# Kernel tuning notes

Hardware: AMD Instinct MI355X
Metric: run time of the kernel (lower is better)

Reference implementation:

```python
import jax, jax.numpy as jnp
import numpy as np


def _graph_conv(x, W, b, src, dst, norm_src, norm_dst, n_nodes):
    # DGL GraphConv, norm='both': out = D_in^{-1/2} * A * D_out^{-1/2} * x * W + b
    h = x * norm_src[:, None]                      # [N, d] scale by src out-degree norm
    m = h[src]                                     # [E, d] gather (irregular access)
    agg = jax.ops.segment_sum(m, dst, num_segments=n_nodes)  # [N, d] scatter-add
    agg = agg * norm_dst[:, None]
    return agg @ W + b


def setup_inputs() -> dict:
    key = jax.random.key(0)
    ks = jax.random.split(key, 6)
    N, E, IN, HID = 50000, 800000, 64, 128
    in_feat = jax.random.normal(ks[0], (N, IN), dtype=jnp.float32)
    W1 = jax.random.normal(ks[1], (IN, HID), dtype=jnp.float32) * (1.0 / np.sqrt(IN))
    b1 = jnp.zeros((HID,), dtype=jnp.float32)
    W2 = jax.random.normal(ks[2], (HID, IN), dtype=jnp.float32) * (1.0 / np.sqrt(HID))
    b2 = jnp.zeros((IN,), dtype=jnp.float32)
    src = jax.random.randint(ks[3], (E,), 0, N, dtype=jnp.int32)
    dst = jax.random.randint(ks[4], (E,), 0, N, dtype=jnp.int32)
    return {"in_feat": in_feat, "W1": W1, "b1": b1, "W2": W2, "b2": b2,
            "src": src, "dst": dst, "n_nodes": N}


def reference(in_feat, W1, b1, W2, b2, src, dst, n_nodes):
    ones = jnp.ones(src.shape, dtype=in_feat.dtype)
    deg_out = jax.ops.segment_sum(ones, src, num_segments=n_nodes)
    deg_in = jax.ops.segment_sum(ones, dst, num_segments=n_nodes)
    # DGL clamps degrees to min 1 (allow_zero_in_degree=True just skips the check)
    norm_src = jnp.clip(deg_out, 1.0, None) ** -0.5
    norm_dst = jnp.clip(deg_in, 1.0, None) ** -0.5
    h = _graph_conv(in_feat, W1, b1, src, dst, norm_src, norm_dst, n_nodes)
    h = jax.nn.relu(h)
    h = _graph_conv(h, W2, b2, src, dst, norm_src, norm_dst, n_nodes)
    return h
```

## Files before the change

### kernel.cpp

```cpp
#include <hip/hip_runtime.h>

#define IN_F 64
#define HID_F 128
#define CAP 64
#define CHUNK 4096
#define CAPB 4096
#define MAXB 512

typedef unsigned short u16;
typedef unsigned int u32;
typedef _Float16 f16;
typedef __attribute__((ext_vector_type(4))) _Float16 f16x4;
typedef __attribute__((ext_vector_type(8))) _Float16 f16x8;
typedef __attribute__((ext_vector_type(4))) float f32x4;

__global__ __launch_bounds__(256)
void partition_kernel(const int* __restrict__ src, const int* __restrict__ dst,
                      int* __restrict__ gcurD, int* __restrict__ gcurS,
                      u32* __restrict__ bufD, u16* __restrict__ bufS,
                      const float* __restrict__ W1, const float* __restrict__ W2,
                      f16* __restrict__ W1t, f16* __restrict__ W2t,
                      int E, int NBUCK) {
    if (blockIdx.x == gridDim.x - 1) {
        for (int t = threadIdx.x; t < 2 * IN_F * HID_F; t += 256) {
            if (t < IN_F * HID_F) {
                int n = t / IN_F, k = t % IN_F;
                W1t[t] = (f16)W1[k * HID_F + n];
            } else {
                int i = t - IN_F * HID_F;
                int n = i / HID_F, k = i % HID_F;
                W2t[i] = (f16)W2[k * IN_F + n];
            }
        }
        return;
    }
    __shared__ int histD[MAXB], histS[MAXB], baseD[MAXB], baseS[MAXB];
    const int t  = threadIdx.x;
    const int e0 = blockIdx.x * CHUNK;
    const int n  = min(CHUNK, E - e0);

    int ed[16], es[16];

    for (int b = t; b < NBUCK; b += 256) { histD[b] = 0; histS[b] = 0; }
    __syncthreads();
#pragma unroll
    for (int j = 0; j < 16; ++j) {
        int i = t + j * 256;
        if (i < n) {
            ed[j] = dst[e0 + i];
            es[j] = src[e0 + i];
            atomicAdd(&histD[ed[j] >> 7], 1);
            atomicAdd(&histS[es[j] >> 7], 1);
        }
    }
    __syncthreads();
    for (int b = t; b < NBUCK; b += 256) {
        baseD[b] = atomicAdd(&gcurD[b], histD[b]);
        baseS[b] = atomicAdd(&gcurS[b], histS[b]);
        histD[b] = 0;
        histS[b] = 0;
    }
    __syncthreads();
#pragma unroll
    for (int j = 0; j < 16; ++j) {
        int i = t + j * 256;
        if (i < n) {
            int d  = ed[j];
            int s  = es[j];
            int bD = d >> 7, bS = s >> 7;
            int p  = baseD[bD] + atomicAdd(&histD[bD], 1);
            if (p < CAPB) bufD[(size_t)bD * CAPB + p] = (u32)d | ((u32)s << 16);
            int p2 = baseS[bS] + atomicAdd(&histS[bS], 1);
            if (p2 < CAPB) bufS[(size_t)bS * CAPB + p2] = (u16)s;
        }
    }
}

__global__ __launch_bounds__(256)
void bucket_pass2_kernel(const u32* __restrict__ bufD, const int* __restrict__ gcurD,
                         const u16* __restrict__ bufS, const int* __restrict__ gcurS,
                         u16* __restrict__ slots, int* __restrict__ deg_in,
                         float* __restrict__ norm_dst, float* __restrict__ norm_src,
                         const float* __restrict__ x, f16x4* __restrict__ scaled_x,
                         int N, int NBUCK) {
    __shared__ int lcur[128];
    const int t = threadIdx.x;
    if (t < 128) lcur[t] = 0;
    __syncthreads();
    if (blockIdx.x < NBUCK) {
        const int b = blockIdx.x;
        const int cnt = min(gcurD[b], CAPB);
        const u32* p = bufD + (size_t)b * CAPB;
        for (int i = t; i < cnt; i += 256) {
            u32 v = p[i];
            int d = (int)(v & 0xFFFFu);
            int s = (int)(v >> 16);
            int pos = atomicAdd(&lcur[d & 127], 1);
            if (pos < CAP) slots[(size_t)d * CAP + pos] = (u16)s;
        }
        __syncthreads();
        int node = b * 128 + t;
        if (t < 128 && node < N) {
            deg_in[node]   = lcur[t];
            norm_dst[node] = rsqrtf((float)max(lcur[t], 1));
        }
    } else {
        const int b = blockIdx.x - NBUCK;
        const int cnt = min(gcurS[b], CAPB);
        const u16* p = bufS + (size_t)b * CAPB;
        for (int i = t; i < cnt; i += 256)
            atomicAdd(&lcur[p[i] & 127], 1);
        __syncthreads();
        int node0 = b * 128;
        if (t < 128 && node0 + t < N)
            norm_src[node0 + t] = rsqrtf((float)max(lcur[t], 1));
        for (int i = t; i < 128 * 16; i += 256) {
            int r = i >> 4, c = i & 15;
            int node = node0 + r;
            if (node < N) {
                float ns = rsqrtf((float)max(lcur[r], 1));
                float4 v = ((const float4*)x)[(size_t)node * 16 + c];
                f16x4 h;
                h.x = (f16)(v.x * ns); h.y = (f16)(v.y * ns);
                h.z = (f16)(v.z * ns); h.w = (f16)(v.w * ns);
                scaled_x[(size_t)node * 16 + c] = h;
            }
        }
    }
}

__global__ __launch_bounds__(256)
void gather_gemm_kernel(const f16x8* __restrict__ xs, const u16* __restrict__ slots,
                        const int* __restrict__ deg_in,
                        const f16* __restrict__ W1t, const float* __restrict__ b1,
                        const float* __restrict__ nd, const float* __restrict__ ns,
                        const f16* __restrict__ W2t, f16* __restrict__ g2, int N) {
    constexpr int LDX = IN_F + 8;
    constexpr int LDH = HID_F + 8;
    __shared__ __align__(16) f16 sx[32 * LDX];
    __shared__ __align__(16) f16 h[2][16 * LDH];

    const int t   = threadIdx.x;
    const int row = t >> 3;
    const int c   = t & 7;
    const int r0  = blockIdx.x * 32;
    const int node = r0 + row;

    float acc[8];
#pragma unroll
    for (int k = 0; k < 8; ++k) acc[k] = 0.f;
    if (node < N) {
        int deg = min(deg_in[node], CAP);
        const u16* srow = slots + (size_t)node * CAP;
        int i = 0;
        for (; i + 8 <= deg; i += 8) {
            int s[8];
#pragma unroll
            for (int j = 0; j < 8; ++j) s[j] = (int)srow[i + j];
            f16x8 v[8];
#pragma unroll
            for (int j = 0; j < 8; ++j) v[j] = xs[(size_t)s[j] * 8 + c];
#pragma unroll
            for (int j = 0; j < 8; ++j)
#pragma unroll
                for (int k = 0; k < 8; ++k) acc[k] += (float)v[j][k];
        }
        for (; i < deg; ++i) {
            f16x8 v = xs[(size_t)srow[i] * 8 + c];
#pragma unroll
            for (int k = 0; k < 8; ++k) acc[k] += (float)v[k];
        }
    }
    {
        f16x8 hv;
#pragma unroll
        for (int k = 0; k < 8; ++k) hv[k] = (f16)acc[k];
        *(f16x8*)&sx[row * LDX + c * 8] = hv;
    }
    __syncthreads();

    const int wave = t >> 6;
    const int lane = t & 63;
    const int nl   = lane & 15;
    const int quad = lane >> 4;

#pragma unroll
    for (int rt = 0; rt < 2; ++rt) {
        f16x8 a1[2];
#pragma unroll
        for (int kf = 0; kf < 2; ++kf)
            a1[kf] = *(const f16x8*)(sx + (rt * 16 + nl) * LDX + kf * 32 + quad * 8);

        float rs1[4];
#pragma unroll
        for (int reg = 0; reg < 4; ++reg)
            rs1[reg] = nd[min(r0 + rt * 16 + quad * 4 + reg, N - 1)];

        f16* hb = h[rt];
#pragma unroll
        for (int cti = 0; cti < 2; ++cti) {
            const int ct = wave * 2 + cti;
            f32x4 acc1 = (f32x4){0.f, 0.f, 0.f, 0.f};
#pragma unroll
            for (int kf = 0; kf < 2; ++kf) {
                f16x8 b = *(const f16x8*)(W1t + (ct * 16 + nl) * IN_F + kf * 32 + quad * 8);
                acc1 = __builtin_amdgcn_mfma_f32_16x16x32_f16(a1[kf], b, acc1, 0, 0, 0);
            }
            float bb = b1[ct * 16 + nl];
#pragma unroll
            for (int reg = 0; reg < 4; ++reg) {
                float v = fmaxf(acc1[reg] * rs1[reg] + bb, 0.f);
                hb[(quad * 4 + reg) * LDH + ct * 16 + nl] = (f16)v;
            }
        }
    }
    __syncthreads();

#pragma unroll
    for (int rt = 0; rt < 2; ++rt) {
        f32x4 acc2 = (f32x4){0.f, 0.f, 0.f, 0.f};
#pragma unroll
        for (int kf = 0; kf < 4; ++kf) {
            f16x8 a2 = *(const f16x8*)(h[rt] + nl * LDH + kf * 32 + quad * 8);
            f16x8 b  = *(const f16x8*)(W2t + (wave * 16 + nl) * HID_F + kf * 32 + quad * 8);
            acc2 = __builtin_amdgcn_mfma_f32_16x16x32_f16(a2, b, acc2, 0, 0, 0);
        }

        float rs2[4];
#pragma unroll
        for (int reg = 0; reg < 4; ++reg)
            rs2[reg] = ns[min(r0 + rt * 16 + quad * 4 + reg, N - 1)];
#pragma unroll
        for (int reg = 0; reg < 4; ++reg) {
            int r = r0 + rt * 16 + quad * 4 + reg;
            if (r < N)
                g2[(size_t)r * IN_F + wave * 16 + nl] = (f16)(acc2[reg] * rs2[reg]);
        }
    }
}

__global__ __launch_bounds__(256)
void gather_out_kernel(const f16x8* __restrict__ xs, const u16* __restrict__ slots,
                       const int* __restrict__ deg_in, const float* __restrict__ sd,
                       const float* __restrict__ bias,
                       float4* __restrict__ out, int N) {
    int tg = blockIdx.x * blockDim.x + threadIdx.x;
    int node = tg >> 3;
    int c = tg & 7;
    if (node >= N) return;
    int deg = min(deg_in[node], CAP);
    const u16* srow = slots + (size_t)node * CAP;
    float acc[8];
#pragma unroll
    for (int k = 0; k < 8; ++k) acc[k] = 0.f;

    int i = 0;
    for (; i + 8 <= deg; i += 8) {
        int s[8];
#pragma unroll
        for (int j = 0; j < 8; ++j) s[j] = (int)srow[i + j];
        f16x8 v[8];
#pragma unroll
        for (int j = 0; j < 8; ++j) v[j] = xs[(size_t)s[j] * 8 + c];
#pragma unroll
        for (int j = 0; j < 8; ++j)
#pragma unroll
            for (int k = 0; k < 8; ++k) acc[k] += (float)v[j][k];
    }
    for (; i < deg; ++i) {
        f16x8 v = xs[(size_t)srow[i] * 8 + c];
#pragma unroll
        for (int k = 0; k < 8; ++k) acc[k] += (float)v[k];
    }
    float d = sd[node];
    float4 b0 = ((const float4*)bias)[c * 2];
    float4 b1v = ((const float4*)bias)[c * 2 + 1];
    float4 o0, o1;
    o0.x = acc[0] * d + b0.x;  o0.y = acc[1] * d + b0.y;
    o0.z = acc[2] * d + b0.z;  o0.w = acc[3] * d + b0.w;
    o1.x = acc[4] * d + b1v.x; o1.y = acc[5] * d + b1v.y;
    o1.z = acc[6] * d + b1v.z; o1.w = acc[7] * d + b1v.w;
    out[(size_t)node * 16 + c * 2]     = o0;
    out[(size_t)node * 16 + c * 2 + 1] = o1;
}

extern "C" void kernel_launch(void* const* d_in, const int* in_sizes, int n_in,
                              void* d_out, int out_size, void* d_ws, size_t ws_size,
                              hipStream_t stream) {
    const float* in_feat = (const float*)d_in[0];
    const float* W1      = (const float*)d_in[1];
    const float* b1      = (const float*)d_in[2];
    const float* W2      = (const float*)d_in[3];
    const float* b2      = (const float*)d_in[4];
    const int*   src     = (const int*)d_in[5];
    const int*   dst     = (const int*)d_in[6];

    const int N = in_sizes[0] / IN_F;
    const int E = in_sizes[5];
    float* out = (float*)d_out;

    const int NBUCK = (N + 127) >> 7;

    int* deg_in  = (int*)d_ws;
    int* gcurD   = deg_in + N;
    int* gcurS   = gcurD + MAXB;
    u16* slots   = (u16*)(gcurS + MAXB);
    float* norm_src = (float*)(slots + (size_t)N * CAP);
    float* norm_dst = norm_src + N;
    f16* scaled_x = (f16*)(norm_dst + N);
    f16* g2       = scaled_x + (size_t)N * IN_F;
    f16* W1t      = g2 + (size_t)N * IN_F;
    f16* W2t      = W1t + IN_F * HID_F;
    u32* bufD     = (u32*)(W2t + IN_F * HID_F);
    u16* bufS     = (u16*)(bufD + (size_t)NBUCK * CAPB);

    hipMemsetAsync(gcurD, 0, sizeof(int) * 2 * MAXB, stream);
    partition_kernel<<<(E + CHUNK - 1) / CHUNK + 1, 256, 0, stream>>>(
        src, dst, gcurD, gcurS, bufD, bufS, W1, W2, W1t, W2t, E, NBUCK);

    bucket_pass2_kernel<<<2 * NBUCK, 256, 0, stream>>>(
        bufD, gcurD, bufS, gcurS, slots, deg_in, norm_dst, norm_src,
        in_feat, (f16x4*)scaled_x, N, NBUCK);

    gather_gemm_kernel<<<(N + 31) / 32, 256, 0, stream>>>(
        (const f16x8*)scaled_x, slots, deg_in, W1t, b1, norm_dst, norm_src,
        W2t, g2, N);

    gather_out_kernel<<<(N * 8 + 255) / 256, 256, 0, stream>>>(
        (const f16x8*)g2, slots, deg_in, norm_dst, b2, (float4*)out, N);
}
```

Before: 167.6 us.

## Replace two-pass bucket partition with direct global-atomic adjacency build

Replaces the bucketed partition and second pass (LDS histograms, staging buffers, bucket scatter) with a single kernel that does global atomicAdd on per-node degree counters and writes the source index straight into the per-destination slot list. A separate prep kernel then computes the norms, writes the scaled fp16 features and transposes the weights. This removes the staging buffers and one full pass over the edges, but adds many contended global atomics with random addresses. Slot order within each node becomes nondeterministic, so fp16 accumulation order varies from run to run.

New measurement: 219.0 us. 1.31x slower.

```diff
diff --git a/kernel.cpp b/kernel.cpp
--- a/kernel.cpp
+++ b/kernel.cpp
@@ -3,9 +3,6 @@
 #define IN_F 64
 #define HID_F 128
 #define CAP 64
-#define CHUNK 4096
-#define CAPB 4096
-#define MAXB 512
 
 typedef unsigned short u16;
 typedef unsigned int u32;
@@ -15,12 +12,39 @@
 typedef __attribute__((ext_vector_type(4))) float f32x4;
 
 __global__ __launch_bounds__(256)
-void partition_kernel(const int* __restrict__ src, const int* __restrict__ dst,
-                      int* __restrict__ gcurD, int* __restrict__ gcurS,
-                      u32* __restrict__ bufD, u16* __restrict__ bufS,
-                      const float* __restrict__ W1, const float* __restrict__ W2,
-                      f16* __restrict__ W1t, f16* __restrict__ W2t,
-                      int E, int NBUCK) {
+void build_kernel(const int* __restrict__ src, const int* __restrict__ dst,
+                  int* __restrict__ deg_in, int* __restrict__ deg_out,
+                  u16* __restrict__ slots, int E) {
+    const int q = blockIdx.x * 256 + threadIdx.x;
+    const int i0 = q * 4;
+    if (i0 + 3 < E) {
+        int4 d4 = ((const int4*)dst)[q];
+        int4 s4 = ((const int4*)src)[q];
+        int dd[4] = {d4.x, d4.y, d4.z, d4.w};
+        int ss[4] = {s4.x, s4.y, s4.z, s4.w};
+#pragma unroll
+        for (int j = 0; j < 4; ++j) {
+            int pos = atomicAdd(&deg_in[dd[j]], 1);
+            if (pos < CAP) slots[(size_t)dd[j] * CAP + pos] = (u16)ss[j];
+            atomicAdd(&deg_out[ss[j]], 1);
+        }
+    } else {
+        for (int i = i0; i < E; ++i) {
+            int d = dst[i], s = src[i];
+            int pos = atomicAdd(&deg_in[d], 1);
+            if (pos < CAP) slots[(size_t)d * CAP + pos] = (u16)s;
+            atomicAdd(&deg_out[s], 1);
+        }
+    }
+}
+
+__global__ __launch_bounds__(256)
+void prep_kernel(const float* __restrict__ x, const int* __restrict__ deg_in,
+                 const int* __restrict__ deg_out,
+                 float* __restrict__ norm_dst, float* __restrict__ norm_src,
+                 f16x8* __restrict__ scaled_x,
+                 const float* __restrict__ W1, const float* __restrict__ W2,
+                 f16* __restrict__ W1t, f16* __restrict__ W2t, int N) {
     if (blockIdx.x == gridDim.x - 1) {
         for (int t = threadIdx.x; t < 2 * IN_F * HID_F; t += 256) {
             if (t < IN_F * HID_F) {
@@ -34,99 +58,23 @@
         }
         return;
     }
-    __shared__ int histD[MAXB], histS[MAXB], baseD[MAXB], baseS[MAXB];
-    const int t  = threadIdx.x;
-    const int e0 = blockIdx.x * CHUNK;
-    const int n  = min(CHUNK, E - e0);
-
-    int ed[16], es[16];
-
-    for (int b = t; b < NBUCK; b += 256) { histD[b] = 0; histS[b] = 0; }
-    __syncthreads();
-#pragma unroll
-    for (int j = 0; j < 16; ++j) {
-        int i = t + j * 256;
-        if (i < n) {
-            ed[j] = dst[e0 + i];
-            es[j] = src[e0 + i];
-            atomicAdd(&histD[ed[j] >> 7], 1);
-            atomicAdd(&histS[es[j] >> 7], 1);
-        }
-    }
-    __syncthreads();
-    for (int b = t; b < NBUCK; b += 256) {
-        baseD[b] = atomicAdd(&gcurD[b], histD[b]);
-        baseS[b] = atomicAdd(&gcurS[b], histS[b]);
-        histD[b] = 0;
-        histS[b] = 0;
-    }
-    __syncthreads();
-#pragma unroll
-    for (int j = 0; j < 16; ++j) {
-        int i = t + j * 256;
-        if (i < n) {
-            int d  = ed[j];
-            int s  = es[j];
-            int bD = d >> 7, bS = s >> 7;
-            int p  = baseD[bD] + atomicAdd(&histD[bD], 1);
-            if (p < CAPB) bufD[(size_t)bD * CAPB + p] = (u32)d | ((u32)s << 16);
-            int p2 = baseS[bS] + atomicAdd(&histS[bS], 1);
-            if (p2 < CAPB) bufS[(size_t)bS * CAPB + p2] = (u16)s;
-        }
-    }
-}
-
-__global__ __launch_bounds__(256)
-void bucket_pass2_kernel(const u32* __restrict__ bufD, const int* __restrict__ gcurD,
-                         const u16* __restrict__ bufS, const int* __restrict__ gcurS,
-                         u16* __restrict__ slots, int* __restrict__ deg_in,
-                         float* __restrict__ norm_dst, float* __restrict__ norm_src,
-                         const float* __restrict__ x, f16x4* __restrict__ scaled_x,
-                         int N, int NBUCK) {
-    __shared__ int lcur[128];
-    const int t = threadIdx.x;
-    if (t < 128) lcur[t] = 0;
-    __syncthreads();
-    if (blockIdx.x < NBUCK) {
-        const int b = blockIdx.x;
-        const int cnt = min(gcurD[b], CAPB);
-        const u32* p = bufD + (size_t)b * CAPB;
-        for (int i = t; i < cnt; i += 256) {
-            u32 v = p[i];
-            int d = (int)(v & 0xFFFFu);
-            int s = (int)(v >> 16);
-            int pos = atomicAdd(&lcur[d & 127], 1);
-            if (pos < CAP) slots[(size_t)d * CAP + pos] = (u16)s;
-        }
-        __syncthreads();
-        int node = b * 128 + t;
-        if (t < 128 && node < N) {
-            deg_in[node]   = lcur[t];
-            norm_dst[node] = rsqrtf((float)max(lcur[t], 1));
-        }
-    } else {
-        const int b = blockIdx.x - NBUCK;
-        const int cnt = min(gcurS[b], CAPB);
-        const u16* p = bufS + (size_t)b * CAPB;
-        for (int i = t; i < cnt; i += 256)
-            atomicAdd(&lcur[p[i] & 127], 1);
-        __syncthreads();
-        int node0 = b * 128;
-        if (t < 128 && node0 + t < N)
-            norm_src[node0 + t] = rsqrtf((float)max(lcur[t], 1));
-        for (int i = t; i < 128 * 16; i += 256) {
-            int r = i >> 4, c = i & 15;
-            int node = node0 + r;
-            if (node < N) {
-                float ns = rsqrtf((float)max(lcur[r], 1));
-                float4 v = ((const float4*)x)[(size_t)node * 16 + c];
-                f16x4 h;
-                h.x = (f16)(v.x * ns); h.y = (f16)(v.y * ns);
-                h.z = (f16)(v.z * ns); h.w = (f16)(v.w * ns);
-                scaled_x[(size_t)node * 16 + c] = h;
-            }
-        }
-    }
+    const int t = blockIdx.x * 256 + threadIdx.x;
+    const int node = t >> 3;
+    const int c = t & 7;
+    if (node >= N) return;
+    float nsv = rsqrtf((float)max(deg_out[node], 1));
+    if (c == 0) {
+        norm_src[node] = nsv;
+        norm_dst[node] = rsqrtf((float)max(deg_in[node], 1));
+    }
+    float4 a = ((const float4*)x)[(size_t)node * 16 + c * 2];
+    float4 b = ((const float4*)x)[(size_t)node * 16 + c * 2 + 1];
+    f16x8 h;
+    h[0] = (f16)(a.x * nsv); h[1] = (f16)(a.y * nsv);
+    h[2] = (f16)(a.z * nsv); h[3] = (f16)(a.w * nsv);
+    h[4] = (f16)(b.x * nsv); h[5] = (f16)(b.y * nsv);
+    h[6] = (f16)(b.z * nsv); h[7] = (f16)(b.w * nsv);
+    scaled_x[(size_t)node * 8 + c] = h;
 }
 
 __global__ __launch_bounds__(256)
@@ -299,28 +247,23 @@
     const int E = in_sizes[5];
     float* out = (float*)d_out;
 
-    const int NBUCK = (N + 127) >> 7;
-
-    int* deg_in  = (int*)d_ws;
-    int* gcurD   = deg_in + N;
-    int* gcurS   = gcurD + MAXB;
-    u16* slots   = (u16*)(gcurS + MAXB);
+    int* deg_in   = (int*)d_ws;
+    int* deg_out  = deg_in + N;
+    u16* slots    = (u16*)(deg_out + N);
     float* norm_src = (float*)(slots + (size_t)N * CAP);
     float* norm_dst = norm_src + N;
     f16* scaled_x = (f16*)(norm_dst + N);
     f16* g2       = scaled_x + (size_t)N * IN_F;
     f16* W1t      = g2 + (size_t)N * IN_F;
     f16* W2t      = W1t + IN_F * HID_F;
-    u32* bufD     = (u32*)(W2t + IN_F * HID_F);
-    u16* bufS     = (u16*)(bufD + (size_t)NBUCK * CAPB);
-
-    hipMemsetAsync(gcurD, 0, sizeof(int) * 2 * MAXB, stream);
-    partition_kernel<<<(E + CHUNK - 1) / CHUNK + 1, 256, 0, stream>>>(
-        src, dst, gcurD, gcurS, bufD, bufS, W1, W2, W1t, W2t, E, NBUCK);
-
-    bucket_pass2_kernel<<<2 * NBUCK, 256, 0, stream>>>(
-        bufD, gcurD, bufS, gcurS, slots, deg_in, norm_dst, norm_src,
-        in_feat, (f16x4*)scaled_x, N, NBUCK);
+
+    hipMemsetAsync(deg_in, 0, sizeof(int) * 2 * N, stream);
+    build_kernel<<<(E / 4 + 255) / 256, 256, 0, stream>>>(
+        src, dst, deg_in, deg_out, slots, E);
+
+    prep_kernel<<<(N * 8 + 255) / 256 + 1, 256, 0, stream>>>(
+        in_feat, deg_in, deg_out, norm_dst, norm_src,
+        (f16x8*)scaled_x, W1, W2, W1t, W2t, N);
 
     gather_gemm_kernel<<<(N + 31) / 32, 256, 0, stream>>>(
         (const f16x8*)scaled_x, slots, deg_in, W1t, b1, norm_dst, norm_src,
```

## Split feature gathers into column halves to shrink random-access working set

Applied to the files above, without the earlier changes.

Stores scaled_x and g2 in a column-split layout of two 32-wide fp16 halves, each contiguous over nodes. Each gather now runs as two passes, one per half, so the randomly accessed table per pass is half the size and more likely to stay in cache. The first layer writes a float32 partial aggregate to a new workspace buffer between passes, and the second layer's output is produced by two kernel launches. Nontemporal loads and stores are used on streamed slots and outputs to keep them from evicting the gathered table, at the cost of reading the slot lists twice and paying extra launches and intermediate traffic.

New measurement: 192.7 us. 1.15x slower.

```diff
diff --git a/kernel.cpp b/kernel.cpp
--- a/kernel.cpp
+++ b/kernel.cpp
@@ -115,26 +115,61 @@
         if (t < 128 && node0 + t < N)
             norm_src[node0 + t] = rsqrtf((float)max(lcur[t], 1));
         for (int i = t; i < 128 * 16; i += 256) {
-            int r = i >> 4, c = i & 15;
+            int r = i >> 4, cc = i & 15;
             int node = node0 + r;
             if (node < N) {
                 float ns = rsqrtf((float)max(lcur[r], 1));
-                float4 v = ((const float4*)x)[(size_t)node * 16 + c];
+                float4 v = ((const float4*)x)[(size_t)node * 16 + cc];
                 f16x4 h;
                 h.x = (f16)(v.x * ns); h.y = (f16)(v.y * ns);
                 h.z = (f16)(v.z * ns); h.w = (f16)(v.w * ns);
-                scaled_x[(size_t)node * 16 + c] = h;
-            }
-        }
-    }
-}
-
-__global__ __launch_bounds__(256)
-void gather_gemm_kernel(const f16x8* __restrict__ xs, const u16* __restrict__ slots,
-                        const int* __restrict__ deg_in,
-                        const f16* __restrict__ W1t, const float* __restrict__ b1,
-                        const float* __restrict__ nd, const float* __restrict__ ns,
-                        const f16* __restrict__ W2t, f16* __restrict__ g2, int N) {
+                scaled_x[((size_t)(cc >> 3) * N + node) * 8 + (cc & 7)] = h;
+            }
+        }
+    }
+}
+
+__global__ __launch_bounds__(256)
+void gather_h0_kernel(const f16x4* __restrict__ xh0, const u16* __restrict__ slots,
+                      const int* __restrict__ deg_in, f32x4* __restrict__ agg0,
+                      int N) {
+    const int t = threadIdx.x;
+    const int row = t >> 3, c = t & 7;
+    const int node = blockIdx.x * 32 + row;
+    if (node >= N) return;
+
+    float acc[4] = {0.f, 0.f, 0.f, 0.f};
+    int deg = min(deg_in[node], CAP);
+    const u16* srow = slots + (size_t)node * CAP;
+    int i = 0;
+    for (; i + 8 <= deg; i += 8) {
+        int s[8];
+#pragma unroll
+        for (int j = 0; j < 8; ++j) s[j] = (int)__builtin_nontemporal_load(&srow[i + j]);
+        f16x4 v[8];
+#pragma unroll
+        for (int j = 0; j < 8; ++j) v[j] = xh0[(size_t)s[j] * 8 + c];
+#pragma unroll
+        for (int j = 0; j < 8; ++j) {
+            acc[0] += (float)v[j].x; acc[1] += (float)v[j].y;
+            acc[2] += (float)v[j].z; acc[3] += (float)v[j].w;
+        }
+    }
+    for (; i < deg; ++i) {
+        f16x4 v = xh0[(size_t)__builtin_nontemporal_load(&srow[i]) * 8 + c];
+        acc[0] += (float)v.x; acc[1] += (float)v.y;
+        acc[2] += (float)v.z; acc[3] += (float)v.w;
+    }
+    f32x4 o = {acc[0], acc[1], acc[2], acc[3]};
+    __builtin_nontemporal_store(o, &agg0[(size_t)node * 8 + c]);
+}
+
+__global__ __launch_bounds__(256)
+void gather_h1_gemm_kernel(const f16x4* __restrict__ xh1, const f32x4* __restrict__ agg0,
+                           const u16* __restrict__ slots, const int* __restrict__ deg_in,
+                           const f16* __restrict__ W1t, const float* __restrict__ b1,
+                           const float* __restrict__ nd, const float* __restrict__ ns,
+                           const f16* __restrict__ W2t, f16* __restrict__ g2, int N) {
     constexpr int LDX = IN_F + 8;
     constexpr int LDH = HID_F + 8;
     __shared__ __align__(16) f16 sx[32 * LDX];
@@ -146,9 +181,7 @@
     const int r0  = blockIdx.x * 32;
     const int node = r0 + row;
 
-    float acc[8];
-#pragma unroll
-    for (int k = 0; k < 8; ++k) acc[k] = 0.f;
+    float acc[4] = {0.f, 0.f, 0.f, 0.f};
     if (node < N) {
         int deg = min(deg_in[node], CAP);
         const u16* srow = slots + (size_t)node * CAP;
@@ -156,26 +189,35 @@
         for (; i + 8 <= deg; i += 8) {
             int s[8];
 #pragma unroll
-            for (int j = 0; j < 8; ++j) s[j] = (int)srow[i + j];
-            f16x8 v[8];
-#pragma unroll
-            for (int j = 0; j < 8; ++j) v[j] = xs[(size_t)s[j] * 8 + c];
-#pragma unroll
-            for (int j = 0; j < 8; ++j)
-#pragma unroll
-                for (int k = 0; k < 8; ++k) acc[k] += (float)v[j][k];
+            for (int j = 0; j < 8; ++j) s[j] = (int)__builtin_nontemporal_load(&srow[i + j]);
+            f16x4 v[8];
+#pragma unroll
+            for (int j = 0; j < 8; ++j) v[j] = xh1[(size_t)s[j] * 8 + c];
+#pragma unroll
+            for (int j = 0; j < 8; ++j) {
+                acc[0] += (float)v[j].x; acc[1] += (float)v[j].y;
+                acc[2] += (float)v[j].z; acc[3] += (float)v[j].w;
+            }
         }
         for (; i < deg; ++i) {
-            f16x8 v = xs[(size_t)srow[i] * 8 + c];
-#pragma unroll
-            for (int k = 0; k < 8; ++k) acc[k] += (float)v[k];
+            f16x4 v = xh1[(size_t)__builtin_nontemporal_load(&srow[i]) * 8 + c];
+            acc[0] += (float)v.x; acc[1] += (float)v.y;
+            acc[2] += (float)v.z; acc[3] += (float)v.w;
         }
     }
     {
-        f16x8 hv;
-#pragma unroll
-        for (int k = 0; k < 8; ++k) hv[k] = (f16)acc[k];
-        *(f16x8*)&sx[row * LDX + c * 8] = hv;
+        f16x4 hv;
+        hv.x = (f16)acc[0]; hv.y = (f16)acc[1];
+        hv.z = (f16)acc[2]; hv.w = (f16)acc[3];
+        *(f16x4*)&sx[row * LDX + 32 + c * 4] = hv;
+    }
+    {
+        f32x4 a0 = {0.f, 0.f, 0.f, 0.f};
+        if (node < N) a0 = __builtin_nontemporal_load(&agg0[(size_t)node * 8 + c]);
+        f16x4 hv;
+        hv.x = (f16)a0.x; hv.y = (f16)a0.y;
+        hv.z = (f16)a0.z; hv.w = (f16)a0.w;
+        *(f16x4*)&sx[row * LDX + c * 4] = hv;
     }
     __syncthreads();
 
@@ -230,58 +272,55 @@
 #pragma unroll
         for (int reg = 0; reg < 4; ++reg)
             rs2[reg] = ns[min(r0 + rt * 16 + quad * 4 + reg, N - 1)];
+        const size_t gbase = ((size_t)(wave >> 1) * N) * 32 + (size_t)((wave & 1) * 16 + nl);
 #pragma unroll
         for (int reg = 0; reg < 4; ++reg) {
             int r = r0 + rt * 16 + quad * 4 + reg;
             if (r < N)
-                g2[(size_t)r * IN_F + wave * 16 + nl] = (f16)(acc2[reg] * rs2[reg]);
-        }
-    }
-}
-
-__global__ __launch_bounds__(256)
-void gather_out_kernel(const f16x8* __restrict__ xs, const u16* __restrict__ slots,
-                       const int* __restrict__ deg_in, const float* __restrict__ sd,
-                       const float* __restrict__ bias,
-                       float4* __restrict__ out, int N) {
+                __builtin_nontemporal_store((f16)(acc2[reg] * rs2[reg]),
+                                            g2 + gbase + (size_t)r * 32);
+        }
+    }
+}
+
+__global__ __launch_bounds__(256)
+void gather_out_h_kernel(const f16x4* __restrict__ g2h, const u16* __restrict__ slots,
+                         const int* __restrict__ deg_in, const float* __restrict__ sd,
+                         const float* __restrict__ bias,
+                         f32x4* __restrict__ out, int N, int hofs) {
     int tg = blockIdx.x * blockDim.x + threadIdx.x;
     int node = tg >> 3;
     int c = tg & 7;
     if (node >= N) return;
     int deg = min(deg_in[node], CAP);
     const u16* srow = slots + (size_t)node * CAP;
-    float acc[8];
-#pragma unroll
-    for (int k = 0; k < 8; ++k) acc[k] = 0.f;
+    float acc[4] = {0.f, 0.f, 0.f, 0.f};
 
     int i = 0;
     for (; i + 8 <= deg; i += 8) {
         int s[8];
 #pragma unroll
-        for (int j = 0; j < 8; ++j) s[j] = (int)srow[i + j];
-        f16x8 v[8];
-#pragma unroll
-        for (int j = 0; j < 8; ++j) v[j] = xs[(size_t)s[j] * 8 + c];
-#pragma unroll
-        for (int j = 0; j < 8; ++j)
-#pragma unroll
-            for (int k = 0; k < 8; ++k) acc[k] += (float)v[j][k];
+        for (int j = 0; j < 8; ++j) s[j] = (int)__builtin_nontemporal_load(&srow[i + j]);
+        f16x4 v[8];
+#pragma unroll
+        for (int j = 0; j < 8; ++j) v[j] = g2h[(size_t)s[j] * 8 + c];
+#pragma unroll
+        for (int j = 0; j < 8; ++j) {
+            acc[0] += (float)v[j].x; acc[1] += (float)v[j].y;
+            acc[2] += (float)v[j].z; acc[3] += (float)v[j].w;
+        }
     }
     for (; i < deg; ++i) {
-        f16x8 v = xs[(size_t)srow[i] * 8 + c];
-#pragma unroll
-        for (int k = 0; k < 8; ++k) acc[k] += (float)v[k];
+        f16x4 v = g2h[(size_t)__builtin_nontemporal_load(&srow[i]) * 8 + c];
+        acc[0] += (float)v.x; acc[1] += (float)v.y;
+        acc[2] += (float)v.z; acc[3] += (float)v.w;
     }
     float d = sd[node];
-    float4 b0 = ((const float4*)bias)[c * 2];
-    float4 b1v = ((const float4*)bias)[c * 2 + 1];
-    float4 o0, o1;
-    o0.x = acc[0] * d + b0.x;  o0.y = acc[1] * d + b0.y;
-    o0.z = acc[2] * d + b0.z;  o0.w = acc[3] * d + b0.w;
-    o1.x = acc[4] * d + b1v.x; o1.y = acc[5] * d + b1v.y;
-    o1.z = acc[6] * d + b1v.z; o1.w = acc[7] * d + b1v.w;
-    out[(size_t)node * 16 + c * 2]     = o0;
-    out[(size_t)node * 16 + c * 2 + 1] = o1;
+    f32x4 bb = ((const f32x4*)bias)[hofs + c];
+    f32x4 o;
+    o.x = acc[0] * d + bb.x; o.y = acc[1] * d + bb.y;
+    o.z = acc[2] * d + bb.z; o.w = acc[3] * d + bb.w;
+    __builtin_nontemporal_store(o, &out[(size_t)node * 16 + hofs + c]);
 }
 
 extern "C" void kernel_launch(void* const* d_in, const int* in_sizes, int n_in,
@@ -313,6 +352,9 @@
     f16* W2t      = W1t + IN_F * HID_F;
     u32* bufD     = (u32*)(W2t + IN_F * HID_F);
     u16* bufS     = (u16*)(bufD + (size_t)NBUCK * CAPB);
+    f32x4* agg0   = (f32x4*)(bufS + (size_t)NBUCK * CAPB);
+
+    const int NB32 = (N + 31) / 32;
 
     hipMemsetAsync(gcurD, 0, sizeof(int) * 2 * MAXB, stream);
     partition_kernel<<<(E + CHUNK - 1) / CHUNK + 1, 256, 0, stream>>>(
@@ -322,10 +364,16 @@
         bufD, gcurD, bufS, gcurS, slots, deg_in, norm_dst, norm_src,
         in_feat, (f16x4*)scaled_x, N, NBUCK);
 
-    gather_gemm_kernel<<<(N + 31) / 32, 256, 0, stream>>>(
-        (const f16x8*)scaled_x, slots, deg_in, W1t, b1, norm_dst, norm_src,
-        W2t, g2, N);
-
-    gather_out_kernel<<<(N * 8 + 255) / 256, 256, 0, stream>>>(
-        (const f16x8*)g2, slots, deg_in, norm_dst, b2, (float4*)out, N);
-}
+    gather_h0_kernel<<<NB32, 256, 0, stream>>>(
+        (const f16x4*)scaled_x, slots, deg_in, agg0, N);
+
+    gather_h1_gemm_kernel<<<NB32, 256, 0, stream>>>(
+        (const f16x4*)(scaled_x + (size_t)N * 32), agg0, slots, deg_in,
+        W1t, b1, norm_dst, norm_src, W2t, g2, N);
+
+    gather_out_h_kernel<<<(N * 8 + 255) / 256, 256, 0, stream>>>(
+        (const f16x4*)g2, slots, deg_in, norm_dst, b2, (f32x4*)out, N, 0);
+    gather_out_h_kernel<<<(N * 8 + 255) / 256, 256, 0, stream>>>(
+        (const f16x4*)(g2 + (size_t)N * 32), slots, deg_in, norm_dst, b2,
+        (f32x4*)out, N, 8);
+}
```
